# Optimization experiments

Hardware: AMD Instinct MI355X
Metric: run time of the kernel (lower is better)

## Reference

```python
import jax, jax.numpy as jnp
import numpy as np

N = 100000      # nodes
E = 1600000     # edges (avg degree 16)
D_IN = 128
H = 256
OUT = 20
EPS = 1e-5      # BatchNorm1d default eps


def setup_inputs() -> dict:
    key = jax.random.key(0)
    ks = jax.random.split(key, 16)
    s = 0.05  # keep activations bounded across stacked layers
    x = jax.random.normal(ks[0], (N, D_IN), jnp.float32)
    edge_index = jax.random.randint(ks[1], (2, E), 0, N, dtype=jnp.int32)
    W0 = jax.random.normal(ks[2], (D_IN, H), jnp.float32) * s
    W1 = jax.random.normal(ks[3], (H, H), jnp.float32) * s
    W2 = jax.random.normal(ks[4], (H, H), jnp.float32) * s
    W3 = jax.random.normal(ks[5], (H, OUT), jnp.float32) * s
    b0 = jnp.zeros((H,), jnp.float32)
    b1 = jnp.zeros((H,), jnp.float32)
    b2 = jnp.zeros((H,), jnp.float32)
    b3 = jnp.zeros((OUT,), jnp.float32)
    gamma = jnp.ones((3, H), jnp.float32) + 0.1 * jax.random.normal(ks[6], (3, H), jnp.float32)
    beta = 0.1 * jax.random.normal(ks[7], (3, H), jnp.float32)
    run_mean = 0.05 * jax.random.normal(ks[8], (3, H), jnp.float32)
    run_var = jnp.ones((3, H), jnp.float32) + 0.5 * jax.random.uniform(ks[9], (3, H), jnp.float32)
    return {"x": x, "edge_index": edge_index,
            "W0": W0, "b0": b0, "W1": W1, "b1": b1, "W2": W2, "b2": b2,
            "W3": W3, "b3": b3, "gamma": gamma, "beta": beta,
            "run_mean": run_mean, "run_var": run_var}


def _gcn_aggregate(h, src, dst, dinv_sqrt):
    # PyG GCNConv: add self-loops, sym-normalized scatter-add of projected feats.
    coef = (dinv_sqrt[src] * dinv_sqrt[dst])[:, None]          # [E,1]
    agg = jax.ops.segment_sum(h[src] * coef, dst, num_segments=N)
    # self-loop contribution: norm = deg^-1 for i==j
    return agg + h * (dinv_sqrt * dinv_sqrt)[:, None]


def reference(x, edge_index, W0, b0, W1, b1, W2, b2, W3, b3,
              gamma, beta, run_mean, run_var):
    src, dst = edge_index[0], edge_index[1]
    # degree with self-loops (counted on dst, as PyG does on col index)
    deg = jax.ops.segment_sum(jnp.ones((E,), jnp.float32), dst, num_segments=N) + 1.0
    dinv_sqrt = jax.lax.rsqrt(deg)

    h = x
    for i, (W, b) in enumerate([(W0, b0), (W1, b1), (W2, b2)]):
        h = _gcn_aggregate(h @ W, src, dst, dinv_sqrt) + b
        # BatchNorm1d in eval mode (running stats), then ReLU; dropout is identity in eval
        h = (h - run_mean[i]) * jax.lax.rsqrt(run_var[i] + EPS) * gamma[i] + beta[i]
        h = jax.nn.relu(h)
    h = _gcn_aggregate(h @ W3, src, dst, dinv_sqrt) + b3
    return h
```

## Files before the change

### kernel.cpp

```cpp
#include <hip/hip_runtime.h>
#include <hip/hip_bf16.h>
#include <stdint.h>

#define NN 100000
#define NE 1600000
#define BNEPS 1e-5f
#define NBKT 391
#define NBA  256
#define CHUNK ((NE + NBA - 1) / NBA)

using short8 = __attribute__((ext_vector_type(8))) short;
using f32x4  = __attribute__((ext_vector_type(4))) float;

__device__ __forceinline__ float b2f(ushort u) {
  union { uint32_t u; float f; } c; c.u = ((uint32_t)u) << 16; return c.f;
}
__device__ __forceinline__ ushort f2bf(float f) {
  union { float f; uint32_t u; } c; c.f = f;
  uint32_t r = (c.u + 0x7FFFu + ((c.u >> 16) & 1u)) >> 16;
  return (ushort)r;
}
__device__ __forceinline__ void gload16(const void* g, void* lds) {
  __builtin_amdgcn_global_load_lds((const __attribute__((address_space(1))) void*)g,
                                   (__attribute__((address_space(3))) void*)lds,
                                   16, 0, 0);
}

__global__ __launch_bounds__(256) void k_hist(const int* __restrict__ dst, int* __restrict__ ghist) {
  __shared__ int h[NBKT];
  for (int t = threadIdx.x; t < NBKT; t += 256) h[t] = 0;
  __syncthreads();
  int e0 = blockIdx.x * CHUNK;
  int e1 = e0 + CHUNK; if (e1 > NE) e1 = NE;
  for (int e = e0 + threadIdx.x; e < e1; e += 256)
    atomicAdd(&h[((uint)dst[e]) >> 8], 1);
  __syncthreads();
  for (int t = threadIdx.x; t < NBKT; t += 256) ghist[t * NBA + blockIdx.x] = h[t];
}

__global__ __launch_bounds__(256) void k_gscanA(const int* __restrict__ ghist, int* __restrict__ gbase,
                                                int* __restrict__ btot) {
  __shared__ int s[256];
  int t = threadIdx.x, b = blockIdx.x;
  int d = ghist[b * NBA + t];
  s[t] = d; __syncthreads();
  int val = d;
  for (int sh = 1; sh < 256; sh <<= 1) {
    int tv = (t >= sh) ? s[t - sh] : 0;
    __syncthreads();
    val += tv; s[t] = val;
    __syncthreads();
  }
  gbase[b * NBA + t] = val - d;
  if (t == 255) btot[b] = val;
}

__global__ __launch_bounds__(512) void k_bscan(const int* __restrict__ btot, int* __restrict__ bbase,
                                               int* __restrict__ offs) {
  __shared__ int s[512];
  int t = threadIdx.x;
  int d = (t < NBKT) ? btot[t] : 0;
  s[t] = d; __syncthreads();
  int val = d;
  for (int sh = 1; sh < 512; sh <<= 1) {
    int tv = (t >= sh) ? s[t - sh] : 0;
    __syncthreads();
    val += tv; s[t] = val;
    __syncthreads();
  }
  if (t < NBKT) bbase[t] = val - d;
  if (t == 0) offs[NN] = NE;
}

__global__ __launch_bounds__(256) void k_scatter(const int* __restrict__ src, const int* __restrict__ dst,
                                                 const int* __restrict__ bbase, const int* __restrict__ gbase,
                                                 uint* __restrict__ bpack) {
  __shared__ int lbase[NBKT];
  for (int t = threadIdx.x; t < NBKT; t += 256)
    lbase[t] = bbase[t] + gbase[t * NBA + blockIdx.x];
  __syncthreads();
  int e0 = blockIdx.x * CHUNK;
  int e1 = e0 + CHUNK; if (e1 > NE) e1 = NE;
  for (int e = e0 + threadIdx.x; e < e1; e += 256) {
    int d = dst[e];
    int pos = atomicAdd(&lbase[((uint)d) >> 8], 1);
    bpack[pos] = ((uint)(d & 255) << 17) | (uint)src[e];
  }
}

__global__ __launch_bounds__(256) void k_bucketB(const uint* __restrict__ bpack, const int* __restrict__ btot,
                                                 const int* __restrict__ bbase, int* __restrict__ csrc,
                                                 int* __restrict__ offs, float* __restrict__ dinv) {
  __shared__ int hist[256];
  __shared__ int sc[256];
  __shared__ int loc[256];
  int b = blockIdx.x, t = threadIdx.x;
  int cnt = btot[b], base = bbase[b];
  const uint* bp = bpack + base;
  hist[t] = 0; __syncthreads();
  for (int i = t; i < cnt; i += 256) atomicAdd(&hist[bp[i] >> 17], 1);
  __syncthreads();
  int d = hist[t];
  sc[t] = d; __syncthreads();
  int val = d;
  for (int sh = 1; sh < 256; sh <<= 1) {
    int tv = (t >= sh) ? sc[t - sh] : 0;
    __syncthreads();
    val += tv; sc[t] = val;
    __syncthreads();
  }
  loc[t] = val - d;
  int n = b * 256 + t;
  if (n < NN) {
    offs[n] = base + val - d;
    dinv[n] = rsqrtf((float)d + 1.0f);
  }
  __syncthreads();
  for (int i = t; i < cnt; i += 256) {
    uint p = bp[i];
    int l = p >> 17, s = p & 0x1FFFF;
    int pos = atomicAdd(&loc[l], 1);
    csrc[base + pos] = s;
  }
}

__global__ __launch_bounds__(256) void k_prep(
    const float* __restrict__ W0, const float* __restrict__ W1, const float* __restrict__ W2,
    const float* __restrict__ W3, const float* __restrict__ b0, const float* __restrict__ b1,
    const float* __restrict__ b2, const float* __restrict__ gamma, const float* __restrict__ beta,
    const float* __restrict__ rm, const float* __restrict__ rv,
    ushort* __restrict__ W0t, ushort* __restrict__ W1t, ushort* __restrict__ W2t,
    ushort* __restrict__ W3t, float* __restrict__ bnA, float* __restrict__ bnB) {
  int tid = blockIdx.x * blockDim.x + threadIdx.x;
  int nthr = gridDim.x * blockDim.x;
  for (int i = tid; i < 256 * 128; i += nthr) { int m = i >> 7, k = i & 127; W0t[i] = f2bf(W0[k * 256 + m]); }
  for (int i = tid; i < 256 * 256; i += nthr) {
    int m = i >> 8, k = i & 255;
    W1t[i] = f2bf(W1[k * 256 + m]);
    W2t[i] = f2bf(W2[k * 256 + m]);
  }
  for (int i = tid; i < 32 * 256; i += nthr) {
    int m = i >> 8, k = i & 255;
    W3t[i] = (m < 20) ? f2bf(W3[k * 20 + m]) : (ushort)0;
  }
  for (int i = tid; i < 3 * 256; i += nthr) {
    int l = i >> 8, c = i & 255;
    float A = gamma[i] * rsqrtf(rv[i] + BNEPS);
    float bb = (l == 0) ? b0[c] : (l == 1) ? b1[c] : b2[c];
    bnA[i] = A;
    bnB[i] = (bb - rm[i]) * A + beta[i];
  }
}

__global__ __launch_bounds__(256) void k_convx(const float4* __restrict__ x, uint2* __restrict__ xb,
                                               const float* __restrict__ dinv) {
  int stride = gridDim.x * blockDim.x;
  const int n4 = NN * 128 / 4;
  for (int i = blockIdx.x * blockDim.x + threadIdx.x; i < n4; i += stride) {
    float4 f = x[i];
    float dv = dinv[i >> 5];
    uint2 o;
    o.x = (uint)f2bf(f.x * dv) | ((uint)f2bf(f.y * dv) << 16);
    o.y = (uint)f2bf(f.z * dv) | ((uint)f2bf(f.w * dv) << 16);
    xb[i] = o;
  }
}

__device__ __forceinline__ void acc2(float* acc, uint2 q) {
  acc[0] += b2f((ushort)(q.x & 0xFFFF));
  acc[1] += b2f((ushort)(q.x >> 16));
  acc[2] += b2f((ushort)(q.y & 0xFFFF));
  acc[3] += b2f((ushort)(q.y >> 16));
}

template<int F, int VEC>
__global__ __launch_bounds__(256) void k_agg(const ushort* __restrict__ Z,
                                             const int* __restrict__ offs, const int* __restrict__ csrc,
                                             const float* __restrict__ dinv, ushort* __restrict__ Outb) {
  int wave = threadIdx.x >> 6, lane = threadIdx.x & 63;
  int v = blockIdx.x * 4 + wave;
  if (v >= NN) return;
  float dv = dinv[v];

  if constexpr (VEC == 4) {
    const uint2* Zq = reinterpret_cast<const uint2*>(Z);
    constexpr int RW = F / 4;
    float acc[4];
    uint2 qs = Zq[(size_t)v * RW + lane];
    acc[0] = b2f((ushort)(qs.x & 0xFFFF));
    acc[1] = b2f((ushort)(qs.x >> 16));
    acc[2] = b2f((ushort)(qs.y & 0xFFFF));
    acc[3] = b2f((ushort)(qs.y >> 16));
    int e = offs[v], e1 = offs[v + 1];
    for (; e + 8 <= e1; e += 8) {
      int u0 = csrc[e + 0], u1 = csrc[e + 1], u2 = csrc[e + 2], u3 = csrc[e + 3];
      int u4 = csrc[e + 4], u5 = csrc[e + 5], u6 = csrc[e + 6], u7 = csrc[e + 7];
      uint2 q0 = Zq[(size_t)u0 * RW + lane];
      uint2 q1 = Zq[(size_t)u1 * RW + lane];
      uint2 q2 = Zq[(size_t)u2 * RW + lane];
      uint2 q3 = Zq[(size_t)u3 * RW + lane];
      uint2 q4 = Zq[(size_t)u4 * RW + lane];
      uint2 q5 = Zq[(size_t)u5 * RW + lane];
      uint2 q6 = Zq[(size_t)u6 * RW + lane];
      uint2 q7 = Zq[(size_t)u7 * RW + lane];
      acc2(acc, q0); acc2(acc, q1); acc2(acc, q2); acc2(acc, q3);
      acc2(acc, q4); acc2(acc, q5); acc2(acc, q6); acc2(acc, q7);
    }
    for (; e + 4 <= e1; e += 4) {
      int u0 = csrc[e + 0], u1 = csrc[e + 1], u2 = csrc[e + 2], u3 = csrc[e + 3];
      uint2 q0 = Zq[(size_t)u0 * RW + lane];
      uint2 q1 = Zq[(size_t)u1 * RW + lane];
      uint2 q2 = Zq[(size_t)u2 * RW + lane];
      uint2 q3 = Zq[(size_t)u3 * RW + lane];
      acc2(acc, q0); acc2(acc, q1); acc2(acc, q2); acc2(acc, q3);
    }
    for (; e < e1; ++e) acc2(acc, Zq[(size_t)csrc[e] * RW + lane]);
    uint2 w;
    w.x = (uint)f2bf(acc[0] * dv) | ((uint)f2bf(acc[1] * dv) << 16);
    w.y = (uint)f2bf(acc[2] * dv) | ((uint)f2bf(acc[3] * dv) << 16);
    reinterpret_cast<uint2*>(Outb)[(size_t)v * RW + lane] = w;
  } else {
    const uint* Zq = reinterpret_cast<const uint*>(Z);
    constexpr int RW = F / 2;
    float acc[2];
    uint qs = Zq[(size_t)v * RW + lane];
    acc[0] = b2f((ushort)(qs & 0xFFFF));
    acc[1] = b2f((ushort)(qs >> 16));
    int e = offs[v], e1 = offs[v + 1];
    for (; e + 4 <= e1; e += 4) {
      int u0 = csrc[e + 0], u1 = csrc[e + 1], u2 = csrc[e + 2], u3 = csrc[e + 3];
      uint q0 = Zq[(size_t)u0 * RW + lane];
      uint q1 = Zq[(size_t)u1 * RW + lane];
      uint q2 = Zq[(size_t)u2 * RW + lane];
      uint q3 = Zq[(size_t)u3 * RW + lane];
      acc[0] += (b2f((ushort)(q0 & 0xFFFF)) + b2f((ushort)(q1 & 0xFFFF)))
              + (b2f((ushort)(q2 & 0xFFFF)) + b2f((ushort)(q3 & 0xFFFF)));
      acc[1] += (b2f((ushort)(q0 >> 16)) + b2f((ushort)(q1 >> 16)))
              + (b2f((ushort)(q2 >> 16)) + b2f((ushort)(q3 >> 16)));
    }
    for (; e < e1; ++e) {
      uint q = Zq[(size_t)csrc[e] * RW + lane];
      acc[0] += b2f((ushort)(q & 0xFFFF));
      acc[1] += b2f((ushort)(q >> 16));
    }
    uint w = (uint)f2bf(acc[0] * dv) | ((uint)f2bf(acc[1] * dv) << 16);
    reinterpret_cast<uint*>(Outb)[(size_t)v * RW + lane] = w;
  }
}

__global__ __launch_bounds__(256) void k_aggfin(const ushort* __restrict__ Z,
                                                const int* __restrict__ offs, const int* __restrict__ csrc,
                                                const float* __restrict__ dinv, const float* __restrict__ b3,
                                                float* __restrict__ out) {
  int wave = threadIdx.x >> 6, lane = threadIdx.x & 63;
  int half = lane >> 5, fl = lane & 31;
  int v = blockIdx.x * 8 + wave * 2 + half;
  if (v >= NN) return;
  float dv = dinv[v];
  float acc = b2f(Z[(size_t)v * 32 + fl]);
  int e = offs[v], e1 = offs[v + 1];
  for (; e + 4 <= e1; e += 4) {
    int u0 = csrc[e + 0], u1 = csrc[e + 1], u2 = csrc[e + 2], u3 = csrc[e + 3];
    float t0 = b2f(Z[(size_t)u0 * 32 + fl]);
    float t1 = b2f(Z[(size_t)u1 * 32 + fl]);
    float t2 = b2f(Z[(size_t)u2 * 32 + fl]);
    float t3 = b2f(Z[(size_t)u3 * 32 + fl]);
    acc += (t0 + t1) + (t2 + t3);
  }
  for (; e < e1; ++e) acc += b2f(Z[(size_t)csrc[e] * 32 + fl]);
  if (fl < 20) out[(size_t)v * 20 + fl] = acc * dv + b3[fl];
}

template<int KTOT, int BN, bool EPI, bool SCALE>
__global__ __launch_bounds__(256) void k_gemm(const ushort* __restrict__ A,
                                              const ushort* __restrict__ Bt,
                                              ushort* __restrict__ Out,
                                              const float* __restrict__ bnA,
                                              const float* __restrict__ bnB,
                                              const float* __restrict__ dinv, int outW) {
  constexpr int BM = 128, BK = 64;
  constexpr int WN = (BN == 128) ? 64 : 16;
  constexpr int WM = 64;
  constexpr int FM = WM / 16, FN = WN / 16;
  __shared__ ushort Alds[BM * BK];
  __shared__ ushort Blds[BN * BK];
  int tid = threadIdx.x;
  int lane = tid & 63;
  int wave = tid >> 6;
  int wm = wave >> 1, wn = wave & 1;
  size_t row0 = (size_t)blockIdx.x * BM;
  int col0 = blockIdx.y * BN;

  f32x4 acc[FM][FN];
#pragma unroll
  for (int i = 0; i < FM; ++i)
#pragma unroll
    for (int j = 0; j < FN; ++j)
#pragma unroll
      for (int r = 0; r < 4; ++r) acc[i][j][r] = 0.0f;

  for (int k0 = 0; k0 < KTOT; k0 += BK) {
#pragma unroll
    for (int is = 0; is < 4; ++is) {
      int idx = is * 256 + tid;
      int r = idx >> 3, c = idx & 7;
      size_t gr = row0 + r; if (gr >= NN) gr = NN - 1;
      gload16(A + gr * KTOT + k0 + c * 8, &Alds[(size_t)(idx & ~63) * 8]);
    }
#pragma unroll
    for (int is = 0; is < BN / 32; ++is) {
      int idx = is * 256 + tid;
      int r = idx >> 3, c = idx & 7;
      gload16(Bt + (size_t)(col0 + r) * KTOT + k0 + c * 8, &Blds[(size_t)(idx & ~63) * 8]);
    }
    __syncthreads();
#pragma unroll
    for (int kk = 0; kk < BK; kk += 32) {
      short8 af[FM]; short8 bfr[FN];
#pragma unroll
      for (int fm = 0; fm < FM; ++fm)
        af[fm] = *reinterpret_cast<const short8*>(&Alds[(wm * WM + fm * 16 + (lane & 15)) * BK + kk + (lane >> 4) * 8]);
#pragma unroll
      for (int fn = 0; fn < FN; ++fn)
        bfr[fn] = *reinterpret_cast<const short8*>(&Blds[(wn * WN + fn * 16 + (lane & 15)) * BK + kk + (lane >> 4) * 8]);
#pragma unroll
      for (int fm = 0; fm < FM; ++fm)
#pragma unroll
        for (int fn = 0; fn < FN; ++fn)
          acc[fm][fn] = __builtin_amdgcn_mfma_f32_16x16x32_bf16(af[fm], bfr[fn], acc[fm][fn], 0, 0, 0);
    }
    __syncthreads();
  }

  int lr = (lane >> 4) * 4, lc = lane & 15;
#pragma unroll
  for (int fm = 0; fm < FM; ++fm) {
#pragma unroll
    for (int r = 0; r < 4; ++r) {
      size_t grow = row0 + wm * WM + fm * 16 + lr + r;
      if (grow >= NN) continue;
      float ds = 1.0f;
      if constexpr (SCALE) ds = dinv[grow];
#pragma unroll
      for (int fn = 0; fn < FN; ++fn) {
        int gcol = col0 + wn * WN + fn * 16 + lc;
        float v = acc[fm][fn][r];
        if constexpr (EPI) v = fmaxf(v * bnA[gcol] + bnB[gcol], 0.0f);
        if constexpr (SCALE) v *= ds;
        Out[grow * outW + gcol] = f2bf(v);
      }
    }
  }
}

extern "C" void kernel_launch(void* const* d_in, const int* in_sizes, int n_in,
                              void* d_out, int out_size, void* d_ws, size_t ws_size,
                              hipStream_t stream) {
  (void)in_sizes; (void)n_in; (void)out_size; (void)ws_size;
  const float* x     = (const float*)d_in[0];
  const int*   ei    = (const int*)d_in[1];
  const float* W0    = (const float*)d_in[2];
  const float* b0    = (const float*)d_in[3];
  const float* W1    = (const float*)d_in[4];
  const float* b1    = (const float*)d_in[5];
  const float* W2    = (const float*)d_in[6];
  const float* b2    = (const float*)d_in[7];
  const float* W3    = (const float*)d_in[8];
  const float* b3    = (const float*)d_in[9];
  const float* gamma = (const float*)d_in[10];
  const float* beta  = (const float*)d_in[11];
  const float* rm    = (const float*)d_in[12];
  const float* rv    = (const float*)d_in[13];
  const int* src = ei;
  const int* dst = ei + NE;
  float* out = (float*)d_out;

  char* ws = (char*)d_ws;
  size_t off = 0;
  auto alloc = [&](size_t bytes) -> void* {
    void* p = ws + off; off += (bytes + 255) & ~(size_t)255; return p;
  };
  int*    ghist = (int*)alloc((size_t)NBKT * NBA * 4);
  int*    gbase = (int*)alloc((size_t)NBKT * NBA * 4);
  int*    btot  = (int*)alloc(NBKT * 4);
  int*    bbase = (int*)alloc(NBKT * 4);
  uint*   bpack = (uint*)alloc((size_t)NE * 4);
  int*    offs  = (int*)alloc((NN + 1) * (size_t)4);
  int*    csrc  = (int*)alloc((size_t)NE * 4);
  float*  dinv  = (float*)alloc(NN * 4);
  ushort* W0t   = (ushort*)alloc(256 * 128 * 2);
  ushort* W1t   = (ushort*)alloc(256 * 256 * 2);
  ushort* W2t   = (ushort*)alloc(256 * 256 * 2);
  ushort* W3t   = (ushort*)alloc(32 * 256 * 2);
  float*  bnA   = (float*)alloc(3 * 256 * 4);
  float*  bnB   = (float*)alloc(3 * 256 * 4);
  ushort* bufS  = (ushort*)alloc((size_t)NN * 128 * 2);
  ushort* bufA  = (ushort*)alloc((size_t)NN * 256 * 2);
  ushort* bufB  = (ushort*)alloc((size_t)NN * 256 * 2);

  k_hist<<<NBA, 256, 0, stream>>>(dst, ghist);
  k_gscanA<<<NBKT, 256, 0, stream>>>(ghist, gbase, btot);
  k_bscan<<<1, 512, 0, stream>>>(btot, bbase, offs);
  k_scatter<<<NBA, 256, 0, stream>>>(src, dst, bbase, gbase, bpack);
  k_bucketB<<<NBKT, 256, 0, stream>>>(bpack, btot, bbase, csrc, offs, dinv);
  k_prep<<<256, 256, 0, stream>>>(W0, W1, W2, W3, b0, b1, b2, gamma, beta, rm, rv,
                                  W0t, W1t, W2t, W3t, bnA, bnB);
  k_convx<<<2048, 256, 0, stream>>>((const float4*)x, (uint2*)bufS, dinv);

  const int aggBlocks = (NN + 3) / 4;
  dim3 gMain((NN + 127) / 128, 2);
  dim3 gLast((NN + 127) / 128, 1);

  k_agg<128, 2><<<aggBlocks, 256, 0, stream>>>(bufS, offs, csrc, dinv, bufA);
  k_gemm<128, 128, true, true><<<gMain, 256, 0, stream>>>(bufA, W0t, bufB, bnA, bnB, dinv, 256);
  k_agg<256, 4><<<aggBlocks, 256, 0, stream>>>(bufB, offs, csrc, dinv, bufA);
  k_gemm<256, 128, true, true><<<gMain, 256, 0, stream>>>(bufA, W1t, bufB, bnA + 256, bnB + 256, dinv, 256);
  k_agg<256, 4><<<aggBlocks, 256, 0, stream>>>(bufB, offs, csrc, dinv, bufA);
  k_gemm<256, 128, true, false><<<gMain, 256, 0, stream>>>(bufA, W2t, bufB, bnA + 512, bnB + 512, nullptr, 256);
  k_gemm<256, 32, false, true><<<gLast, 256, 0, stream>>>(bufB, W3t, bufS, nullptr, nullptr, dinv, 32);
  k_aggfin<<<(NN + 7) / 8, 256, 0, stream>>>(bufS, offs, csrc, dinv, b3, out);
}
```

Baseline: 530.2 us.

## Split neighbor lists across lane groups with 16-byte gathers in aggregation kernels

The three gather/aggregate kernels are restructured so each wave splits a node's edge list across 2, 4 or 8 lane groups. Each group loads whole feature rows with wider 16-byte (or 8-byte) vector loads, and the partial sums are combined with cross-lane shuffles. This is meant to increase memory-level parallelism and use wider loads for the scattered row gathers, and to stop most of a wave idling on the narrow final layer. In exchange it adds shuffle reductions, more registers per lane, and a changed output-lane mapping in the writes.

```diff
diff --git a/kernel.cpp b/kernel.cpp
--- a/kernel.cpp
+++ b/kernel.cpp
@@ -20,10 +20,25 @@
   uint32_t r = (c.u + 0x7FFFu + ((c.u >> 16) & 1u)) >> 16;
   return (ushort)r;
 }
+__device__ __forceinline__ uint pk(float a, float b) {
+  return (uint)f2bf(a) | ((uint)f2bf(b) << 16);
+}
 __device__ __forceinline__ void gload16(const void* g, void* lds) {
   __builtin_amdgcn_global_load_lds((const __attribute__((address_space(1))) void*)g,
                                    (__attribute__((address_space(3))) void*)lds,
                                    16, 0, 0);
+}
+__device__ __forceinline__ void add16(float* a, uint4 q) {
+  a[0] += b2f((ushort)(q.x & 0xFFFF)); a[1] += b2f((ushort)(q.x >> 16));
+  a[2] += b2f((ushort)(q.y & 0xFFFF)); a[3] += b2f((ushort)(q.y >> 16));
+  a[4] += b2f((ushort)(q.z & 0xFFFF)); a[5] += b2f((ushort)(q.z >> 16));
+  a[6] += b2f((ushort)(q.w & 0xFFFF)); a[7] += b2f((ushort)(q.w >> 16));
+}
+__device__ __forceinline__ void set16(float* a, uint4 q) {
+  a[0] = b2f((ushort)(q.x & 0xFFFF)); a[1] = b2f((ushort)(q.x >> 16));
+  a[2] = b2f((ushort)(q.y & 0xFFFF)); a[3] = b2f((ushort)(q.y >> 16));
+  a[4] = b2f((ushort)(q.z & 0xFFFF)); a[5] = b2f((ushort)(q.z >> 16));
+  a[6] = b2f((ushort)(q.w & 0xFFFF)); a[7] = b2f((ushort)(q.w >> 16));
 }
 
 __global__ __launch_bounds__(256) void k_hist(const int* __restrict__ dst, int* __restrict__ ghist) {
@@ -160,92 +175,83 @@
     float4 f = x[i];
     float dv = dinv[i >> 5];
     uint2 o;
-    o.x = (uint)f2bf(f.x * dv) | ((uint)f2bf(f.y * dv) << 16);
-    o.y = (uint)f2bf(f.z * dv) | ((uint)f2bf(f.w * dv) << 16);
+    o.x = pk(f.x * dv, f.y * dv);
+    o.y = pk(f.z * dv, f.w * dv);
     xb[i] = o;
   }
 }
 
-__device__ __forceinline__ void acc2(float* acc, uint2 q) {
-  acc[0] += b2f((ushort)(q.x & 0xFFFF));
-  acc[1] += b2f((ushort)(q.x >> 16));
-  acc[2] += b2f((ushort)(q.y & 0xFFFF));
-  acc[3] += b2f((ushort)(q.y >> 16));
-}
-
-template<int F, int VEC>
-__global__ __launch_bounds__(256) void k_agg(const ushort* __restrict__ Z,
-                                             const int* __restrict__ offs, const int* __restrict__ csrc,
-                                             const float* __restrict__ dinv, ushort* __restrict__ Outb) {
+
+__global__ __launch_bounds__(256) void k_agg256(const ushort* __restrict__ Z,
+                                                const int* __restrict__ offs, const int* __restrict__ csrc,
+                                                const float* __restrict__ dinv, ushort* __restrict__ Outb) {
   int wave = threadIdx.x >> 6, lane = threadIdx.x & 63;
   int v = blockIdx.x * 4 + wave;
   if (v >= NN) return;
   float dv = dinv[v];
-
-  if constexpr (VEC == 4) {
-    const uint2* Zq = reinterpret_cast<const uint2*>(Z);
-    constexpr int RW = F / 4;
-    float acc[4];
-    uint2 qs = Zq[(size_t)v * RW + lane];
-    acc[0] = b2f((ushort)(qs.x & 0xFFFF));
-    acc[1] = b2f((ushort)(qs.x >> 16));
-    acc[2] = b2f((ushort)(qs.y & 0xFFFF));
-    acc[3] = b2f((ushort)(qs.y >> 16));
-    int e = offs[v], e1 = offs[v + 1];
-    for (; e + 8 <= e1; e += 8) {
-      int u0 = csrc[e + 0], u1 = csrc[e + 1], u2 = csrc[e + 2], u3 = csrc[e + 3];
-      int u4 = csrc[e + 4], u5 = csrc[e + 5], u6 = csrc[e + 6], u7 = csrc[e + 7];
-      uint2 q0 = Zq[(size_t)u0 * RW + lane];
-      uint2 q1 = Zq[(size_t)u1 * RW + lane];
-      uint2 q2 = Zq[(size_t)u2 * RW + lane];
-      uint2 q3 = Zq[(size_t)u3 * RW + lane];
-      uint2 q4 = Zq[(size_t)u4 * RW + lane];
-      uint2 q5 = Zq[(size_t)u5 * RW + lane];
-      uint2 q6 = Zq[(size_t)u6 * RW + lane];
-      uint2 q7 = Zq[(size_t)u7 * RW + lane];
-      acc2(acc, q0); acc2(acc, q1); acc2(acc, q2); acc2(acc, q3);
-      acc2(acc, q4); acc2(acc, q5); acc2(acc, q6); acc2(acc, q7);
-    }
-    for (; e + 4 <= e1; e += 4) {
-      int u0 = csrc[e + 0], u1 = csrc[e + 1], u2 = csrc[e + 2], u3 = csrc[e + 3];
-      uint2 q0 = Zq[(size_t)u0 * RW + lane];
-      uint2 q1 = Zq[(size_t)u1 * RW + lane];
-      uint2 q2 = Zq[(size_t)u2 * RW + lane];
-      uint2 q3 = Zq[(size_t)u3 * RW + lane];
-      acc2(acc, q0); acc2(acc, q1); acc2(acc, q2); acc2(acc, q3);
-    }
-    for (; e < e1; ++e) acc2(acc, Zq[(size_t)csrc[e] * RW + lane]);
-    uint2 w;
-    w.x = (uint)f2bf(acc[0] * dv) | ((uint)f2bf(acc[1] * dv) << 16);
-    w.y = (uint)f2bf(acc[2] * dv) | ((uint)f2bf(acc[3] * dv) << 16);
-    reinterpret_cast<uint2*>(Outb)[(size_t)v * RW + lane] = w;
+  int p = lane >> 5, fl = lane & 31;
+  const uint4* Z4 = reinterpret_cast<const uint4*>(Z);
+  float acc[8];
+  if (p == 0) {
+    set16(acc, Z4[(size_t)v * 32 + fl]);
   } else {
-    const uint* Zq = reinterpret_cast<const uint*>(Z);
-    constexpr int RW = F / 2;
-    float acc[2];
-    uint qs = Zq[(size_t)v * RW + lane];
-    acc[0] = b2f((ushort)(qs & 0xFFFF));
-    acc[1] = b2f((ushort)(qs >> 16));
-    int e = offs[v], e1 = offs[v + 1];
-    for (; e + 4 <= e1; e += 4) {
-      int u0 = csrc[e + 0], u1 = csrc[e + 1], u2 = csrc[e + 2], u3 = csrc[e + 3];
-      uint q0 = Zq[(size_t)u0 * RW + lane];
-      uint q1 = Zq[(size_t)u1 * RW + lane];
-      uint q2 = Zq[(size_t)u2 * RW + lane];
-      uint q3 = Zq[(size_t)u3 * RW + lane];
-      acc[0] += (b2f((ushort)(q0 & 0xFFFF)) + b2f((ushort)(q1 & 0xFFFF)))
-              + (b2f((ushort)(q2 & 0xFFFF)) + b2f((ushort)(q3 & 0xFFFF)));
-      acc[1] += (b2f((ushort)(q0 >> 16)) + b2f((ushort)(q1 >> 16)))
-              + (b2f((ushort)(q2 >> 16)) + b2f((ushort)(q3 >> 16)));
-    }
-    for (; e < e1; ++e) {
-      uint q = Zq[(size_t)csrc[e] * RW + lane];
-      acc[0] += b2f((ushort)(q & 0xFFFF));
-      acc[1] += b2f((ushort)(q >> 16));
-    }
-    uint w = (uint)f2bf(acc[0] * dv) | ((uint)f2bf(acc[1] * dv) << 16);
-    reinterpret_cast<uint*>(Outb)[(size_t)v * RW + lane] = w;
-  }
+#pragma unroll
+    for (int j = 0; j < 8; ++j) acc[j] = 0.0f;
+  }
+  int e1 = offs[v + 1];
+  int e = offs[v] + p;
+  for (; e + 6 < e1; e += 8) {
+    int u0 = csrc[e], u1 = csrc[e + 2], u2 = csrc[e + 4], u3 = csrc[e + 6];
+    uint4 q0 = Z4[(size_t)u0 * 32 + fl];
+    uint4 q1 = Z4[(size_t)u1 * 32 + fl];
+    uint4 q2 = Z4[(size_t)u2 * 32 + fl];
+    uint4 q3 = Z4[(size_t)u3 * 32 + fl];
+    add16(acc, q0); add16(acc, q1); add16(acc, q2); add16(acc, q3);
+  }
+  for (; e < e1; e += 2) add16(acc, Z4[(size_t)csrc[e] * 32 + fl]);
+#pragma unroll
+  for (int j = 0; j < 8; ++j) acc[j] += __shfl_xor(acc[j], 32);
+  int o = p * 4;
+  uint2 w;
+  w.x = pk(acc[o + 0] * dv, acc[o + 1] * dv);
+  w.y = pk(acc[o + 2] * dv, acc[o + 3] * dv);
+  reinterpret_cast<uint2*>(Outb)[(size_t)v * 64 + fl * 2 + p] = w;
+}
+
+__global__ __launch_bounds__(256) void k_agg128(const ushort* __restrict__ Z,
+                                                const int* __restrict__ offs, const int* __restrict__ csrc,
+                                                const float* __restrict__ dinv, ushort* __restrict__ Outb) {
+  int wave = threadIdx.x >> 6, lane = threadIdx.x & 63;
+  int v = blockIdx.x * 4 + wave;
+  if (v >= NN) return;
+  float dv = dinv[v];
+  int q = lane >> 4, fl = lane & 15;
+  const uint4* Z4 = reinterpret_cast<const uint4*>(Z);
+  float acc[8];
+  if (q == 0) {
+    set16(acc, Z4[(size_t)v * 16 + fl]);
+  } else {
+#pragma unroll
+    for (int j = 0; j < 8; ++j) acc[j] = 0.0f;
+  }
+  int e1 = offs[v + 1];
+  int e = offs[v] + q;
+  for (; e + 12 < e1; e += 16) {
+    int u0 = csrc[e], u1 = csrc[e + 4], u2 = csrc[e + 8], u3 = csrc[e + 12];
+    uint4 q0 = Z4[(size_t)u0 * 16 + fl];
+    uint4 q1 = Z4[(size_t)u1 * 16 + fl];
+    uint4 q2 = Z4[(size_t)u2 * 16 + fl];
+    uint4 q3 = Z4[(size_t)u3 * 16 + fl];
+    add16(acc, q0); add16(acc, q1); add16(acc, q2); add16(acc, q3);
+  }
+  for (; e < e1; e += 4) add16(acc, Z4[(size_t)csrc[e] * 16 + fl]);
+#pragma unroll
+  for (int j = 0; j < 8; ++j) {
+    acc[j] += __shfl_xor(acc[j], 16);
+    acc[j] += __shfl_xor(acc[j], 32);
+  }
+  uint w = pk(acc[2 * q] * dv, acc[2 * q + 1] * dv);
+  reinterpret_cast<uint*>(Outb)[(size_t)v * 64 + fl * 4 + q] = w;
 }
 
 __global__ __launch_bounds__(256) void k_aggfin(const ushort* __restrict__ Z,
@@ -253,22 +259,49 @@
                                                 const float* __restrict__ dinv, const float* __restrict__ b3,
                                                 float* __restrict__ out) {
   int wave = threadIdx.x >> 6, lane = threadIdx.x & 63;
-  int half = lane >> 5, fl = lane & 31;
-  int v = blockIdx.x * 8 + wave * 2 + half;
+  int v = blockIdx.x * 4 + wave;
   if (v >= NN) return;
   float dv = dinv[v];
-  float acc = b2f(Z[(size_t)v * 32 + fl]);
-  int e = offs[v], e1 = offs[v + 1];
-  for (; e + 4 <= e1; e += 4) {
-    int u0 = csrc[e + 0], u1 = csrc[e + 1], u2 = csrc[e + 2], u3 = csrc[e + 3];
-    float t0 = b2f(Z[(size_t)u0 * 32 + fl]);
-    float t1 = b2f(Z[(size_t)u1 * 32 + fl]);
-    float t2 = b2f(Z[(size_t)u2 * 32 + fl]);
-    float t3 = b2f(Z[(size_t)u3 * 32 + fl]);
-    acc += (t0 + t1) + (t2 + t3);
-  }
-  for (; e < e1; ++e) acc += b2f(Z[(size_t)csrc[e] * 32 + fl]);
-  if (fl < 20) out[(size_t)v * 20 + fl] = acc * dv + b3[fl];
+  int s = lane >> 3, fl = lane & 7;
+  const uint2* Z2 = reinterpret_cast<const uint2*>(Z);
+  float acc[4];
+  if (s == 0) {
+    uint2 qq = Z2[(size_t)v * 8 + fl];
+    acc[0] = b2f((ushort)(qq.x & 0xFFFF)); acc[1] = b2f((ushort)(qq.x >> 16));
+    acc[2] = b2f((ushort)(qq.y & 0xFFFF)); acc[3] = b2f((ushort)(qq.y >> 16));
+  } else {
+    acc[0] = acc[1] = acc[2] = acc[3] = 0.0f;
+  }
+  int e1 = offs[v + 1];
+  int e = offs[v] + s;
+  for (; e + 8 < e1; e += 16) {
+    int u0 = csrc[e], u1 = csrc[e + 8];
+    uint2 q0 = Z2[(size_t)u0 * 8 + fl];
+    uint2 q1 = Z2[(size_t)u1 * 8 + fl];
+    acc[0] += b2f((ushort)(q0.x & 0xFFFF)) + b2f((ushort)(q1.x & 0xFFFF));
+    acc[1] += b2f((ushort)(q0.x >> 16))    + b2f((ushort)(q1.x >> 16));
+    acc[2] += b2f((ushort)(q0.y & 0xFFFF)) + b2f((ushort)(q1.y & 0xFFFF));
+    acc[3] += b2f((ushort)(q0.y >> 16))    + b2f((ushort)(q1.y >> 16));
+  }
+  for (; e < e1; e += 8) {
+    uint2 qq = Z2[(size_t)csrc[e] * 8 + fl];
+    acc[0] += b2f((ushort)(qq.x & 0xFFFF)); acc[1] += b2f((ushort)(qq.x >> 16));
+    acc[2] += b2f((ushort)(qq.y & 0xFFFF)); acc[3] += b2f((ushort)(qq.y >> 16));
+  }
+#pragma unroll
+  for (int j = 0; j < 4; ++j) {
+    acc[j] += __shfl_xor(acc[j], 8);
+    acc[j] += __shfl_xor(acc[j], 16);
+    acc[j] += __shfl_xor(acc[j], 32);
+  }
+  if (s == 0 && fl < 5) {
+    float4 w;
+    w.x = acc[0] * dv + b3[fl * 4 + 0];
+    w.y = acc[1] * dv + b3[fl * 4 + 1];
+    w.z = acc[2] * dv + b3[fl * 4 + 2];
+    w.w = acc[3] * dv + b3[fl * 4 + 3];
+    *reinterpret_cast<float4*>(out + (size_t)v * 20 + fl * 4) = w;
+  }
 }
 
 template<int KTOT, int BN, bool EPI, bool SCALE>
@@ -411,12 +444,12 @@
   dim3 gMain((NN + 127) / 128, 2);
   dim3 gLast((NN + 127) / 128, 1);
 
-  k_agg<128, 2><<<aggBlocks, 256, 0, stream>>>(bufS, offs, csrc, dinv, bufA);
+  k_agg128<<<aggBlocks, 256, 0, stream>>>(bufS, offs, csrc, dinv, bufA);
   k_gemm<128, 128, true, true><<<gMain, 256, 0, stream>>>(bufA, W0t, bufB, bnA, bnB, dinv, 256);
-  k_agg<256, 4><<<aggBlocks, 256, 0, stream>>>(bufB, offs, csrc, dinv, bufA);
+  k_agg256<<<aggBlocks, 256, 0, stream>>>(bufB, offs, csrc, dinv, bufA);
   k_gemm<256, 128, true, true><<<gMain, 256, 0, stream>>>(bufA, W1t, bufB, bnA + 256, bnB + 256, dinv, 256);
-  k_agg<256, 4><<<aggBlocks, 256, 0, stream>>>(bufB, offs, csrc, dinv, bufA);
+  k_agg256<<<aggBlocks, 256, 0, stream>>>(bufB, offs, csrc, dinv, bufA);
   k_gemm<256, 128, true, false><<<gMain, 256, 0, stream>>>(bufA, W2t, bufB, bnA + 512, bnB + 512, nullptr, 256);
   k_gemm<256, 32, false, true><<<gLast, 256, 0, stream>>>(bufB, W3t, bufS, nullptr, nullptr, dinv, 32);
-  k_aggfin<<<(NN + 7) / 8, 256, 0, stream>>>(bufS, offs, csrc, dinv, b3, out);
-}
+  k_aggfin<<<aggBlocks, 256, 0, stream>>>(bufS, offs, csrc, dinv, b3, out);
+}
```

New measurement: 526.4 us. Within noise of the previous version (-0.7%).
